# Kernel tuning notes

Measured on AMD Instinct MI355X. Metric: run time of the kernel, lower is better.

## Reference

```python
import jax, jax.numpy as jnp
import numpy as np

N_NODES = 100000
N_EDGES = 3200000


def _gcn_conv(x, src, dst, W, b, n_nodes):
    # PyG GCNConv: out = D^{-1/2} (A + I) D^{-1/2} X W + b
    h = x @ W  # [N, out]
    # degree of (A + I) counted at targets (symmetric graph assumption as in PyG norm)
    deg = jax.ops.segment_sum(jnp.ones_like(dst, dtype=h.dtype), dst, num_segments=n_nodes)
    dinv = jnp.where(deg > 0, jax.lax.rsqrt(deg), 0.0)
    norm = dinv[src] * dinv[dst]  # [E_total]
    msg = h[src] * norm[:, None]  # gather + normalize  [E_total, out]
    out = jax.ops.segment_sum(msg, dst, num_segments=n_nodes)  # scatter-add
    return out + b


def setup_inputs() -> dict:
    key = jax.random.key(0)
    k1, k2, k3, k4 = jax.random.split(key, 4)
    x = jax.random.normal(k1, (N_NODES, 1), dtype=jnp.float32)
    edge_index = jax.random.randint(k2, (2, N_EDGES), 0, N_NODES, dtype=jnp.int64)
    W1 = jax.random.normal(k3, (1, 64), dtype=jnp.float32) * (1.0 / np.sqrt(1.0))
    b1 = jnp.zeros((64,), dtype=jnp.float32)
    W2 = jax.random.normal(k4, (64, 2), dtype=jnp.float32) * (1.0 / np.sqrt(64.0))
    b2 = jnp.zeros((2,), dtype=jnp.float32)
    return {"x": x, "edge_index": edge_index, "W1": W1, "b1": b1, "W2": W2, "b2": b2}


def reference(x, edge_index, W1, b1, W2, b2):
    n = x.shape[0]
    # add self-loops as GCNConv does by default
    loops = jnp.arange(n, dtype=edge_index.dtype)
    src = jnp.concatenate([edge_index[0], loops])
    dst = jnp.concatenate([edge_index[1], loops])
    h = _gcn_conv(x, src, dst, W1, b1, n)
    h = jax.nn.relu(h)
    h = _gcn_conv(h, src, dst, W2, b2, n)
    h = jax.nn.log_softmax(h, axis=1)
    out = jnp.mean(h, axis=0)
    return out[None, :]  # [1, 2]
```

## Files before the change

### kernel.cpp

```cpp
#include <hip/hip_runtime.h>


#define TPB 512
#define SORT_BLK 256
#define BSHIFT 7
#define BNODES 128
#define MAXBUCK 1024
#define BSTRIDE 6144


__global__ __launch_bounds__(TPB) void k_sort(const int* __restrict__ ei, int E, int epb,
                                              int nbuck, int* __restrict__ gcur,
                                              unsigned* __restrict__ packed) {
    __shared__ int h[MAXBUCK];
    for (int b = threadIdx.x; b < nbuck; b += TPB) h[b] = 0;
    __syncthreads();
    const int4* d4 = (const int4*)(ei + E);
    int nq = epb >> 2;
    int q0 = blockIdx.x * nq;
    for (int j = threadIdx.x; j < nq; j += TPB) {
        int q = q0 + j;
        int e = q << 2;
        if (e + 3 < E) {
            int4 v = d4[q];
            atomicAdd(&h[v.x >> BSHIFT], 1);
            atomicAdd(&h[v.y >> BSHIFT], 1);
            atomicAdd(&h[v.z >> BSHIFT], 1);
            atomicAdd(&h[v.w >> BSHIFT], 1);
        } else {
            for (int k = 0; k < 4; ++k)
                if (e + k < E) atomicAdd(&h[(ei + E)[e + k] >> BSHIFT], 1);
        }
    }
    __syncthreads();
    for (int b = threadIdx.x; b < nbuck; b += TPB) {
        int c = h[b];
        h[b] = c ? atomicAdd(&gcur[b], c) : 0;
    }
    __syncthreads();
    const int4* s4 = (const int4*)ei;
    for (int j = threadIdx.x; j < nq; j += TPB) {
        int q = q0 + j;
        int e = q << 2;
        if (e + 3 < E) {
            int4 vs = s4[q];
            int4 vd = d4[q];
            int b, p;
            b = vd.x >> BSHIFT; p = atomicAdd(&h[b], 1);
            packed[b * BSTRIDE + p] = ((unsigned)(vd.x & (BNODES - 1)) << 17) | (unsigned)vs.x;
            b = vd.y >> BSHIFT; p = atomicAdd(&h[b], 1);
            packed[b * BSTRIDE + p] = ((unsigned)(vd.y & (BNODES - 1)) << 17) | (unsigned)vs.y;
            b = vd.z >> BSHIFT; p = atomicAdd(&h[b], 1);
            packed[b * BSTRIDE + p] = ((unsigned)(vd.z & (BNODES - 1)) << 17) | (unsigned)vs.z;
            b = vd.w >> BSHIFT; p = atomicAdd(&h[b], 1);
            packed[b * BSTRIDE + p] = ((unsigned)(vd.w & (BNODES - 1)) << 17) | (unsigned)vs.w;
        } else {
            for (int k = 0; k < 4; ++k) {
                int ee = e + k;
                if (ee < E) {
                    int s = ei[ee], d = ei[E + ee];
                    int b = d >> BSHIFT;
                    int p = atomicAdd(&h[b], 1);
                    packed[b * BSTRIDE + p] = ((unsigned)(d & (BNODES - 1)) << 17) | (unsigned)s;
                }
            }
        }
    }
}


__global__ __launch_bounds__(TPB) void k_csr(unsigned* __restrict__ packed,
                                             const int* __restrict__ gcur,
                                             const float* __restrict__ x,
                                             float* __restrict__ dinv,
                                             float* __restrict__ u,
                                             int* __restrict__ rptr, int N) {
    __shared__ int cnt[8][BNODES];
    __shared__ int eptr[BNODES];
    __shared__ unsigned stage[BSTRIDE];
    for (int k = threadIdx.x; k < 8 * BNODES; k += TPB) ((int*)cnt)[k] = 0;
    __syncthreads();
    int b = blockIdx.x;
    int sz = gcur[b];
    unsigned* base = packed + (size_t)b * BSTRIDE;
    const uint4* base4 = (const uint4*)base;
    int wv = threadIdx.x >> 6;
    int nq4 = sz >> 2;
    int half = nq4 >> 1;
    for (int j = threadIdx.x; j < half; j += TPB) {
        uint4 p = base4[j];
        uint4 q = base4[j + half];
        atomicAdd(&cnt[wv][(p.x >> 17) & 127], 1);
        atomicAdd(&cnt[wv][(p.y >> 17) & 127], 1);
        atomicAdd(&cnt[wv][(p.z >> 17) & 127], 1);
        atomicAdd(&cnt[wv][(p.w >> 17) & 127], 1);
        atomicAdd(&cnt[wv][(q.x >> 17) & 127], 1);
        atomicAdd(&cnt[wv][(q.y >> 17) & 127], 1);
        atomicAdd(&cnt[wv][(q.z >> 17) & 127], 1);
        atomicAdd(&cnt[wv][(q.w >> 17) & 127], 1);
    }
    for (int j = half * 8 + threadIdx.x; j < sz; j += TPB) {
        unsigned p = base[j];
        atomicAdd(&cnt[wv][(p >> 17) & 127], 1);
    }
    __syncthreads();
    int tot = 0;
    if (threadIdx.x < BNODES) {
        #pragma unroll
        for (int c = 0; c < 8; ++c) tot += cnt[c][threadIdx.x];
        eptr[threadIdx.x] = tot;
    }
    __syncthreads();
    for (int d = 1; d < BNODES; d <<= 1) {
        int add = 0;
        if (threadIdx.x < BNODES && threadIdx.x >= d) add = eptr[threadIdx.x - d];
        __syncthreads();
        if (threadIdx.x < BNODES) eptr[threadIdx.x] += add;
        __syncthreads();
    }
    if (threadIdx.x < BNODES) {
        int t = threadIdx.x;
        int ex = eptr[t] - tot;
        int run = ex;
        #pragma unroll
        for (int c = 0; c < 8; ++c) { int v = cnt[c][t]; cnt[c][t] = run; run += v; }
        rptr[b * BNODES + t] = ex;
        int node = (b << BSHIFT) + t;
        if (node < N) {
            float di = rsqrtf((float)(tot + 1));
            dinv[node] = di;
            u[node] = di * x[node];
        }
    }
    __syncthreads();
    for (int j = threadIdx.x; j < half; j += TPB) {
        uint4 p = base4[j];
        uint4 q = base4[j + half];
        int pos;
        pos = atomicAdd(&cnt[wv][(p.x >> 17) & 127], 1); stage[pos] = p.x & 0x1FFFF;
        pos = atomicAdd(&cnt[wv][(p.y >> 17) & 127], 1); stage[pos] = p.y & 0x1FFFF;
        pos = atomicAdd(&cnt[wv][(p.z >> 17) & 127], 1); stage[pos] = p.z & 0x1FFFF;
        pos = atomicAdd(&cnt[wv][(p.w >> 17) & 127], 1); stage[pos] = p.w & 0x1FFFF;
        pos = atomicAdd(&cnt[wv][(q.x >> 17) & 127], 1); stage[pos] = q.x & 0x1FFFF;
        pos = atomicAdd(&cnt[wv][(q.y >> 17) & 127], 1); stage[pos] = q.y & 0x1FFFF;
        pos = atomicAdd(&cnt[wv][(q.z >> 17) & 127], 1); stage[pos] = q.z & 0x1FFFF;
        pos = atomicAdd(&cnt[wv][(q.w >> 17) & 127], 1); stage[pos] = q.w & 0x1FFFF;
    }
    for (int j = half * 8 + threadIdx.x; j < sz; j += TPB) {
        unsigned p = base[j];
        int pos = atomicAdd(&cnt[wv][(p >> 17) & 127], 1);
        stage[pos] = p & 0x1FFFF;
    }
    __syncthreads();
    for (int k = threadIdx.x; k < sz; k += TPB) base[k] = stage[k];
}


__global__ __launch_bounds__(TPB) void k_agg1(const unsigned* __restrict__ sorted,
                                              const int* __restrict__ gcur,
                                              const int* __restrict__ rptr,
                                              const float* __restrict__ dinv,
                                              const float* __restrict__ u,
                                              const float* __restrict__ W1,
                                              const float* __restrict__ b1,
                                              const float* __restrict__ W2,
                                              float2* __restrict__ w, int N) {
    __shared__ float sW1[64], sb1[64], sW2[128];
    __shared__ int sptr[BNODES + 1];
    int b = blockIdx.x;
    if (threadIdx.x < 64) { sW1[threadIdx.x] = W1[threadIdx.x]; sb1[threadIdx.x] = b1[threadIdx.x]; }
    else if (threadIdx.x < 192) sW2[threadIdx.x - 64] = W2[threadIdx.x - 64];
    if (threadIdx.x < BNODES) sptr[threadIdx.x] = rptr[b * BNODES + threadIdx.x];
    if (threadIdx.x == 0) sptr[BNODES] = gcur[b];
    __syncthreads();
    int t = threadIdx.x >> 2, k = threadIdx.x & 3;
    const unsigned* base = sorted + (size_t)b * BSTRIDE;
    int s0 = sptr[t], s1 = sptr[t + 1];
    float s = 0.f;
    int j = s0 + k;
    for (; j + 12 < s1; j += 16) {
        unsigned i0 = base[j], i1 = base[j + 4], i2 = base[j + 8], i3 = base[j + 12];
        float a0 = u[i0], a1 = u[i1], a2 = u[i2], a3 = u[i3];
        s += (a0 + a1) + (a2 + a3);
    }
    for (; j < s1; j += 4) s += u[base[j]];
    s += __shfl_xor(s, 1, 64);
    s += __shfl_xor(s, 2, 64);
    int node = (b << BSHIFT) + t;
    if (k == 0 && node < N) {
        float di = dinv[node];
        float sv = di * (s + u[node]);
        float z0 = 0.f, z1 = 0.f;
        #pragma unroll
        for (int jj = 0; jj < 64; ++jj) {
            float h = fmaxf(fmaf(sv, sW1[jj], sb1[jj]), 0.f);
            z0 = fmaf(h, sW2[2 * jj], z0);
            z1 = fmaf(h, sW2[2 * jj + 1], z1);
        }
        w[node] = make_float2(di * z0, di * z1);
    }
}


__global__ __launch_bounds__(TPB) void k_agg2(const unsigned* __restrict__ sorted,
                                              const int* __restrict__ gcur,
                                              const int* __restrict__ rptr,
                                              const float* __restrict__ dinv,
                                              const float2* __restrict__ w,
                                              const float* __restrict__ b2,
                                              float* __restrict__ accum, int N) {
    __shared__ int sptr[BNODES + 1];
    int b = blockIdx.x;
    if (threadIdx.x < BNODES) sptr[threadIdx.x] = rptr[b * BNODES + threadIdx.x];
    if (threadIdx.x == 0) sptr[BNODES] = gcur[b];
    __syncthreads();
    int t = threadIdx.x >> 2, k = threadIdx.x & 3;
    const unsigned* base = sorted + (size_t)b * BSTRIDE;
    int s0 = sptr[t], s1 = sptr[t + 1];
    float sx = 0.f, sy = 0.f;
    int j = s0 + k;
    for (; j + 12 < s1; j += 16) {
        unsigned i0 = base[j], i1 = base[j + 4], i2 = base[j + 8], i3 = base[j + 12];
        float2 v0 = w[i0], v1 = w[i1], v2 = w[i2], v3 = w[i3];
        sx += (v0.x + v1.x) + (v2.x + v3.x);
        sy += (v0.y + v1.y) + (v2.y + v3.y);
    }
    for (; j < s1; j += 4) {
        float2 v = w[base[j]];
        sx += v.x;
        sy += v.y;
    }
    sx += __shfl_xor(sx, 1, 64); sx += __shfl_xor(sx, 2, 64);
    sy += __shfl_xor(sy, 1, 64); sy += __shfl_xor(sy, 2, 64);
    int node = (b << BSHIFT) + t;
    float l0 = 0.f, l1 = 0.f;
    if (k == 0 && node < N) {
        float di = dinv[node];
        float2 wi = w[node];
        float a0 = di * (sx + wi.x) + b2[0];
        float a1 = di * (sy + wi.y) + b2[1];
        float m = fmaxf(a0, a1);
        float lse = m + logf(expf(a0 - m) + expf(a1 - m));
        l0 = a0 - lse;
        l1 = a1 - lse;
    }
    #pragma unroll
    for (int off = 32; off > 0; off >>= 1) {
        l0 += __shfl_down(l0, off, 64);
        l1 += __shfl_down(l1, off, 64);
    }
    __shared__ float r0[TPB / 64], r1[TPB / 64];
    int wid = threadIdx.x >> 6, lane = threadIdx.x & 63;
    if (lane == 0) { r0[wid] = l0; r1[wid] = l1; }
    __syncthreads();
    if (threadIdx.x == 0) {
        float t0 = 0.f, t1 = 0.f;
        #pragma unroll
        for (int kk = 0; kk < TPB / 64; ++kk) { t0 += r0[kk]; t1 += r1[kk]; }
        accum[2 * b]     = t0;
        accum[2 * b + 1] = t1;
    }
}


#define RTPB 1024
__global__ __launch_bounds__(RTPB) void k_reduce_final(const float* __restrict__ accum,
                                                       int nb, float* __restrict__ out,
                                                       float invN) {
    float t0 = 0.f, t1 = 0.f;
    for (int i = threadIdx.x; i < nb; i += RTPB) {
        t0 += accum[2 * i];
        t1 += accum[2 * i + 1];
    }
    #pragma unroll
    for (int off = 32; off > 0; off >>= 1) {
        t0 += __shfl_down(t0, off, 64);
        t1 += __shfl_down(t1, off, 64);
    }
    __shared__ float s0[RTPB / 64], s1[RTPB / 64];
    int wid = threadIdx.x >> 6, lane = threadIdx.x & 63;
    if (lane == 0) { s0[wid] = t0; s1[wid] = t1; }
    __syncthreads();
    if (threadIdx.x == 0) {
        float a = 0.f, b = 0.f;
        #pragma unroll
        for (int k = 0; k < RTPB / 64; ++k) { a += s0[k]; b += s1[k]; }
        out[0] = a * invN;
        out[1] = b * invN;
    }
}

__global__ void k_finalize(const float* __restrict__ accum, float* __restrict__ out, float invN) {
    out[0] = accum[0] * invN;
    out[1] = accum[1] * invN;
}


#define FTPB 256
__global__ void k_hist(const int* __restrict__ dst, int E, int* __restrict__ deg) {
    int e = blockIdx.x * FTPB + threadIdx.x;
    if (e < E) atomicAdd(&deg[dst[e]], 1);
}
__global__ void k_dinv_u(const int* __restrict__ deg, const float* __restrict__ x,
                         float* __restrict__ dinv, float* __restrict__ u, int N) {
    int i = blockIdx.x * FTPB + threadIdx.x;
    if (i < N) {
        float di = rsqrtf((float)(deg[i] + 1));
        dinv[i] = di;
        u[i] = di * x[i];
    }
}
__global__ void k_scatter1(const int* __restrict__ ei, int E,
                           const float* __restrict__ u, float* __restrict__ t) {
    int e = blockIdx.x * FTPB + threadIdx.x;
    if (e < E) atomicAdd(&t[ei[E + e]], u[ei[e]]);
}
__global__ void k_node_mid_fb(const float* __restrict__ dinv, const float* __restrict__ u,
                              const float* __restrict__ t,
                              const float* __restrict__ W1, const float* __restrict__ b1,
                              const float* __restrict__ W2, float2* __restrict__ w, int N) {
    __shared__ float sW1[64], sb1[64], sW2[128];
    if (threadIdx.x < 64) { sW1[threadIdx.x] = W1[threadIdx.x]; sb1[threadIdx.x] = b1[threadIdx.x]; }
    if (threadIdx.x < 128) sW2[threadIdx.x] = W2[threadIdx.x];
    __syncthreads();
    int i = blockIdx.x * FTPB + threadIdx.x;
    if (i < N) {
        float di = dinv[i];
        float s = di * (t[i] + u[i]);
        float z0 = 0.f, z1 = 0.f;
        #pragma unroll
        for (int j = 0; j < 64; ++j) {
            float h = fmaxf(fmaf(s, sW1[j], sb1[j]), 0.f);
            z0 = fmaf(h, sW2[2 * j], z0);
            z1 = fmaf(h, sW2[2 * j + 1], z1);
        }
        w[i] = make_float2(di * z0, di * z1);
    }
}
__global__ void k_scatter2(const int* __restrict__ ei, int E,
                           const float2* __restrict__ w, float* __restrict__ acc) {
    int e = blockIdx.x * FTPB + threadIdx.x;
    if (e < E) {
        float2 ws = w[ei[e]];
        int d = ei[E + e];
        atomicAdd(&acc[2 * d], ws.x);
        atomicAdd(&acc[2 * d + 1], ws.y);
    }
}
__global__ void k_node_out_fb(const float* __restrict__ dinv, const float2* __restrict__ w,
                              const float2* __restrict__ acc, const float* __restrict__ b2,
                              float* __restrict__ accum, int N) {
    int i = blockIdx.x * FTPB + threadIdx.x;
    float l0 = 0.f, l1 = 0.f;
    if (i < N) {
        float di = dinv[i];
        float2 a = acc[i];
        float2 ww = w[i];
        float a0 = di * (a.x + ww.x) + b2[0];
        float a1 = di * (a.y + ww.y) + b2[1];
        float m = fmaxf(a0, a1);
        float lse = m + logf(expf(a0 - m) + expf(a1 - m));
        l0 = a0 - lse;
        l1 = a1 - lse;
    }
    #pragma unroll
    for (int off = 32; off > 0; off >>= 1) {
        l0 += __shfl_down(l0, off, 64);
        l1 += __shfl_down(l1, off, 64);
    }
    __shared__ float s0[FTPB / 64], s1[FTPB / 64];
    int wid = threadIdx.x >> 6, lane = threadIdx.x & 63;
    if (lane == 0) { s0[wid] = l0; s1[wid] = l1; }
    __syncthreads();
    if (threadIdx.x == 0) {
        float t0 = 0.f, t1 = 0.f;
        #pragma unroll
        for (int k = 0; k < FTPB / 64; ++k) { t0 += s0[k]; t1 += s1[k]; }
        atomicAdd(&accum[0], t0);
        atomicAdd(&accum[1], t1);
    }
}

extern "C" void kernel_launch(void* const* d_in, const int* in_sizes, int n_in,
                              void* d_out, int out_size, void* d_ws, size_t ws_size,
                              hipStream_t stream) {
    const float* x  = (const float*)d_in[0];
    const int*   ei = (const int*)d_in[1];
    const float* W1 = (const float*)d_in[2];
    const float* b1 = (const float*)d_in[3];
    const float* W2 = (const float*)d_in[4];
    const float* b2 = (const float*)d_in[5];
    float* out = (float*)d_out;

    const int N = in_sizes[0];
    const int E = in_sizes[1] / 2;
    const int nbuck = (N + BNODES - 1) >> BSHIFT;
    const int gridN = (N + FTPB - 1) / FTPB;
    const int gridE = (E + FTPB - 1) / FTPB;

    size_t offPacked = 0;
    size_t offW      = offPacked + (size_t)nbuck * BSTRIDE * 4;
    size_t offDinv   = offW + (size_t)N * 8;
    size_t offU      = offDinv + (size_t)N * 4;
    size_t offGcur   = offU + (size_t)N * 4;
    size_t offAccum  = offGcur + (size_t)nbuck * 4;
    size_t offRptr   = offAccum + (size_t)2 * nbuck * 4;
    size_t need      = offRptr + (size_t)nbuck * BNODES * 4;

    if (ws_size >= need && nbuck <= MAXBUCK && N <= (1 << 17)) {
        unsigned* packed = (unsigned*)((char*)d_ws + offPacked);
        float2*   w      = (float2*)((char*)d_ws + offW);
        float*    dinv   = (float*)((char*)d_ws + offDinv);
        float*    u      = (float*)((char*)d_ws + offU);
        int*      gcur   = (int*)((char*)d_ws + offGcur);
        float*    accum  = (float*)((char*)d_ws + offAccum);
        int*      rptr   = (int*)((char*)d_ws + offRptr);

        hipMemsetAsync(gcur, 0, (size_t)nbuck * 4, stream);

        int epb = (((E + SORT_BLK - 1) / SORT_BLK) + 3) & ~3;

        k_sort<<<SORT_BLK, TPB, 0, stream>>>(ei, E, epb, nbuck, gcur, packed);
        k_csr<<<nbuck, TPB, 0, stream>>>(packed, gcur, x, dinv, u, rptr, N);
        k_agg1<<<nbuck, TPB, 0, stream>>>(packed, gcur, rptr, dinv, u, W1, b1, W2, w, N);
        k_agg2<<<nbuck, TPB, 0, stream>>>(packed, gcur, rptr, dinv, (const float2*)w, b2, accum, N);
        k_reduce_final<<<1, RTPB, 0, stream>>>(accum, nbuck, out, 1.0f / (float)N);
    } else {
        int*   deg   = (int*)d_ws;
        float* t     = (float*)(deg + N);
        float* acc   = t + N;
        float* accum = acc + 2 * N;
        float* dinv  = accum + 2;
        float* u     = dinv + N;
        float2* w    = (float2*)(u + N);
        hipMemsetAsync(d_ws, 0, (size_t)(4 * N + 2) * sizeof(float), stream);
        k_hist<<<gridE, FTPB, 0, stream>>>(ei + E, E, deg);
        k_dinv_u<<<gridN, FTPB, 0, stream>>>(deg, x, dinv, u, N);
        k_scatter1<<<gridE, FTPB, 0, stream>>>(ei, E, u, t);
        k_node_mid_fb<<<gridN, FTPB, 0, stream>>>(dinv, u, t, W1, b1, W2, w, N);
        k_scatter2<<<gridE, FTPB, 0, stream>>>(ei, E, w, acc);
        k_node_out_fb<<<gridN, FTPB, 0, stream>>>(dinv, w, (const float2*)acc, b2, accum, N);
        k_finalize<<<1, 64, 0, stream>>>(accum, out, 1.0f / (float)N);
    }
}
```

Before: 160.9 us.

## Cache CSR bucket data in registers, warp-scan offsets, unroll gathers, fuse final reduction

k_csr now loads each bucket's packed edges into registers once and reuses them for both the counting and scatter passes, instead of reading global memory twice. Its 128-entry scan becomes a wavefront shuffle scan, which cuts the many block-wide barriers. The gather loops in both aggregation kernels are unrolled to 8 outstanding loads per lane for more memory-level parallelism. The separate final-reduction kernel is replaced by a last-block-done pattern inside k_agg2, with an atomic counter and fences, which saves one launch but adds atomics and a serial tail in one block.

```diff
diff --git a/kernel.cpp b/kernel.cpp
--- a/kernel.cpp
+++ b/kernel.cpp
@@ -7,6 +7,10 @@
 #define BNODES 128
 #define MAXBUCK 1024
 #define BSTRIDE 6144
+
+__device__ __forceinline__ float ld_dev_f32(const float* p) {
+    return __hip_atomic_load(p, __ATOMIC_RELAXED, __HIP_MEMORY_SCOPE_AGENT);
+}
 
 
 __global__ __launch_bounds__(TPB) void k_sort(const int* __restrict__ ei, int E, int epb,
@@ -78,54 +82,75 @@
     __shared__ int cnt[8][BNODES];
     __shared__ int eptr[BNODES];
     __shared__ unsigned stage[BSTRIDE];
-    for (int k = threadIdx.x; k < 8 * BNODES; k += TPB) ((int*)cnt)[k] = 0;
-    __syncthreads();
-    int b = blockIdx.x;
-    int sz = gcur[b];
+    const int tid = threadIdx.x;
+    for (int k = tid; k < 8 * BNODES; k += TPB) ((int*)cnt)[k] = 0;
+    __syncthreads();
+    const int b = blockIdx.x;
+    const int sz = gcur[b];
     unsigned* base = packed + (size_t)b * BSTRIDE;
     const uint4* base4 = (const uint4*)base;
-    int wv = threadIdx.x >> 6;
-    int nq4 = sz >> 2;
-    int half = nq4 >> 1;
-    for (int j = threadIdx.x; j < half; j += TPB) {
-        uint4 p = base4[j];
-        uint4 q = base4[j + half];
-        atomicAdd(&cnt[wv][(p.x >> 17) & 127], 1);
-        atomicAdd(&cnt[wv][(p.y >> 17) & 127], 1);
-        atomicAdd(&cnt[wv][(p.z >> 17) & 127], 1);
-        atomicAdd(&cnt[wv][(p.w >> 17) & 127], 1);
-        atomicAdd(&cnt[wv][(q.x >> 17) & 127], 1);
-        atomicAdd(&cnt[wv][(q.y >> 17) & 127], 1);
-        atomicAdd(&cnt[wv][(q.z >> 17) & 127], 1);
-        atomicAdd(&cnt[wv][(q.w >> 17) & 127], 1);
-    }
-    for (int j = half * 8 + threadIdx.x; j < sz; j += TPB) {
-        unsigned p = base[j];
-        atomicAdd(&cnt[wv][(p >> 17) & 127], 1);
-    }
+    const int wv = tid >> 6;
+    const int nq4 = sz >> 2;
+    const int half = nq4 >> 1;
+    uint4 rp[2], rq[2];
+    int nit = 0;
+    #pragma unroll
+    for (int it = 0; it < 2; ++it) {
+        int j = tid + it * TPB;
+        if (j < half) {
+            rp[it] = base4[j];
+            rq[it] = base4[j + half];
+            nit = it + 1;
+        }
+    }
+    unsigned rt = 0; int havet = 0;
+    {
+        int j = half * 8 + tid;
+        if (j < sz) { rt = base[j]; havet = 1; }
+    }
+    #pragma unroll
+    for (int it = 0; it < 2; ++it) {
+        if (it < nit) {
+            uint4 p = rp[it], q = rq[it];
+            atomicAdd(&cnt[wv][(p.x >> 17) & 127], 1);
+            atomicAdd(&cnt[wv][(p.y >> 17) & 127], 1);
+            atomicAdd(&cnt[wv][(p.z >> 17) & 127], 1);
+            atomicAdd(&cnt[wv][(p.w >> 17) & 127], 1);
+            atomicAdd(&cnt[wv][(q.x >> 17) & 127], 1);
+            atomicAdd(&cnt[wv][(q.y >> 17) & 127], 1);
+            atomicAdd(&cnt[wv][(q.z >> 17) & 127], 1);
+            atomicAdd(&cnt[wv][(q.w >> 17) & 127], 1);
+        }
+    }
+    if (havet) atomicAdd(&cnt[wv][(rt >> 17) & 127], 1);
     __syncthreads();
     int tot = 0;
-    if (threadIdx.x < BNODES) {
-        #pragma unroll
-        for (int c = 0; c < 8; ++c) tot += cnt[c][threadIdx.x];
-        eptr[threadIdx.x] = tot;
-    }
-    __syncthreads();
-    for (int d = 1; d < BNODES; d <<= 1) {
-        int add = 0;
-        if (threadIdx.x < BNODES && threadIdx.x >= d) add = eptr[threadIdx.x - d];
-        __syncthreads();
-        if (threadIdx.x < BNODES) eptr[threadIdx.x] += add;
-        __syncthreads();
-    }
-    if (threadIdx.x < BNODES) {
-        int t = threadIdx.x;
-        int ex = eptr[t] - tot;
+    if (tid < BNODES) {
+        #pragma unroll
+        for (int c = 0; c < 8; ++c) tot += cnt[c][tid];
+        eptr[tid] = tot;
+    }
+    __syncthreads();
+    if (tid < 64) {
+        int v0 = eptr[tid], v1 = eptr[tid + 64];
+        #pragma unroll
+        for (int off = 1; off < 64; off <<= 1) {
+            int t0 = __shfl_up(v0, off, 64);
+            int t1 = __shfl_up(v1, off, 64);
+            if (tid >= off) { v0 += t0; v1 += t1; }
+        }
+        v1 += __shfl(v0, 63, 64);
+        eptr[tid] = v0;
+        eptr[tid + 64] = v1;
+    }
+    __syncthreads();
+    if (tid < BNODES) {
+        int ex = eptr[tid] - tot;
         int run = ex;
         #pragma unroll
-        for (int c = 0; c < 8; ++c) { int v = cnt[c][t]; cnt[c][t] = run; run += v; }
-        rptr[b * BNODES + t] = ex;
-        int node = (b << BSHIFT) + t;
+        for (int c = 0; c < 8; ++c) { int v = cnt[c][tid]; cnt[c][tid] = run; run += v; }
+        rptr[b * BNODES + tid] = ex;
+        int node = (b << BSHIFT) + tid;
         if (node < N) {
             float di = rsqrtf((float)(tot + 1));
             dinv[node] = di;
@@ -133,26 +158,27 @@
         }
     }
     __syncthreads();
-    for (int j = threadIdx.x; j < half; j += TPB) {
-        uint4 p = base4[j];
-        uint4 q = base4[j + half];
-        int pos;
-        pos = atomicAdd(&cnt[wv][(p.x >> 17) & 127], 1); stage[pos] = p.x & 0x1FFFF;
-        pos = atomicAdd(&cnt[wv][(p.y >> 17) & 127], 1); stage[pos] = p.y & 0x1FFFF;
-        pos = atomicAdd(&cnt[wv][(p.z >> 17) & 127], 1); stage[pos] = p.z & 0x1FFFF;
-        pos = atomicAdd(&cnt[wv][(p.w >> 17) & 127], 1); stage[pos] = p.w & 0x1FFFF;
-        pos = atomicAdd(&cnt[wv][(q.x >> 17) & 127], 1); stage[pos] = q.x & 0x1FFFF;
-        pos = atomicAdd(&cnt[wv][(q.y >> 17) & 127], 1); stage[pos] = q.y & 0x1FFFF;
-        pos = atomicAdd(&cnt[wv][(q.z >> 17) & 127], 1); stage[pos] = q.z & 0x1FFFF;
-        pos = atomicAdd(&cnt[wv][(q.w >> 17) & 127], 1); stage[pos] = q.w & 0x1FFFF;
-    }
-    for (int j = half * 8 + threadIdx.x; j < sz; j += TPB) {
-        unsigned p = base[j];
-        int pos = atomicAdd(&cnt[wv][(p >> 17) & 127], 1);
-        stage[pos] = p & 0x1FFFF;
-    }
-    __syncthreads();
-    for (int k = threadIdx.x; k < sz; k += TPB) base[k] = stage[k];
+    #pragma unroll
+    for (int it = 0; it < 2; ++it) {
+        if (it < nit) {
+            uint4 p = rp[it], q = rq[it];
+            int pos;
+            pos = atomicAdd(&cnt[wv][(p.x >> 17) & 127], 1); stage[pos] = p.x & 0x1FFFF;
+            pos = atomicAdd(&cnt[wv][(p.y >> 17) & 127], 1); stage[pos] = p.y & 0x1FFFF;
+            pos = atomicAdd(&cnt[wv][(p.z >> 17) & 127], 1); stage[pos] = p.z & 0x1FFFF;
+            pos = atomicAdd(&cnt[wv][(p.w >> 17) & 127], 1); stage[pos] = p.w & 0x1FFFF;
+            pos = atomicAdd(&cnt[wv][(q.x >> 17) & 127], 1); stage[pos] = q.x & 0x1FFFF;
+            pos = atomicAdd(&cnt[wv][(q.y >> 17) & 127], 1); stage[pos] = q.y & 0x1FFFF;
+            pos = atomicAdd(&cnt[wv][(q.z >> 17) & 127], 1); stage[pos] = q.z & 0x1FFFF;
+            pos = atomicAdd(&cnt[wv][(q.w >> 17) & 127], 1); stage[pos] = q.w & 0x1FFFF;
+        }
+    }
+    if (havet) {
+        int pos = atomicAdd(&cnt[wv][(rt >> 17) & 127], 1);
+        stage[pos] = rt & 0x1FFFF;
+    }
+    __syncthreads();
+    for (int k = tid; k < sz; k += TPB) base[k] = stage[k];
 }
 
 
@@ -178,6 +204,13 @@
     int s0 = sptr[t], s1 = sptr[t + 1];
     float s = 0.f;
     int j = s0 + k;
+    for (; j + 28 < s1; j += 32) {
+        unsigned i0 = base[j],      i1 = base[j + 4],  i2 = base[j + 8],  i3 = base[j + 12];
+        unsigned i4 = base[j + 16], i5 = base[j + 20], i6 = base[j + 24], i7 = base[j + 28];
+        float a0 = u[i0], a1 = u[i1], a2 = u[i2], a3 = u[i3];
+        float a4 = u[i4], a5 = u[i5], a6 = u[i6], a7 = u[i7];
+        s += ((a0 + a1) + (a2 + a3)) + ((a4 + a5) + (a6 + a7));
+    }
     for (; j + 12 < s1; j += 16) {
         unsigned i0 = base[j], i1 = base[j + 4], i2 = base[j + 8], i3 = base[j + 12];
         float a0 = u[i0], a1 = u[i1], a2 = u[i2], a3 = u[i3];
@@ -208,17 +241,31 @@
                                               const float* __restrict__ dinv,
                                               const float2* __restrict__ w,
                                               const float* __restrict__ b2,
-                                              float* __restrict__ accum, int N) {
+                                              float* __restrict__ accum,
+                                              int* __restrict__ done,
+                                              float* __restrict__ out,
+                                              int nbuck, float invN, int N) {
     __shared__ int sptr[BNODES + 1];
+    __shared__ float r0[TPB / 64], r1[TPB / 64];
+    __shared__ int lastFlag;
+    const int tid = threadIdx.x;
     int b = blockIdx.x;
-    if (threadIdx.x < BNODES) sptr[threadIdx.x] = rptr[b * BNODES + threadIdx.x];
-    if (threadIdx.x == 0) sptr[BNODES] = gcur[b];
-    __syncthreads();
-    int t = threadIdx.x >> 2, k = threadIdx.x & 3;
+    if (tid < BNODES) sptr[tid] = rptr[b * BNODES + tid];
+    if (tid == 0) sptr[BNODES] = gcur[b];
+    __syncthreads();
+    int t = tid >> 2, k = tid & 3;
     const unsigned* base = sorted + (size_t)b * BSTRIDE;
     int s0 = sptr[t], s1 = sptr[t + 1];
     float sx = 0.f, sy = 0.f;
     int j = s0 + k;
+    for (; j + 28 < s1; j += 32) {
+        unsigned i0 = base[j],      i1 = base[j + 4],  i2 = base[j + 8],  i3 = base[j + 12];
+        unsigned i4 = base[j + 16], i5 = base[j + 20], i6 = base[j + 24], i7 = base[j + 28];
+        float2 v0 = w[i0], v1 = w[i1], v2 = w[i2], v3 = w[i3];
+        float2 v4 = w[i4], v5 = w[i5], v6 = w[i6], v7 = w[i7];
+        sx += ((v0.x + v1.x) + (v2.x + v3.x)) + ((v4.x + v5.x) + (v6.x + v7.x));
+        sy += ((v0.y + v1.y) + (v2.y + v3.y)) + ((v4.y + v5.y) + (v6.y + v7.y));
+    }
     for (; j + 12 < s1; j += 16) {
         unsigned i0 = base[j], i1 = base[j + 4], i2 = base[j + 8], i3 = base[j + 12];
         float2 v0 = w[i0], v1 = w[i1], v2 = w[i2], v3 = w[i3];
@@ -249,44 +296,41 @@
         l0 += __shfl_down(l0, off, 64);
         l1 += __shfl_down(l1, off, 64);
     }
-    __shared__ float r0[TPB / 64], r1[TPB / 64];
-    int wid = threadIdx.x >> 6, lane = threadIdx.x & 63;
+    int wid = tid >> 6, lane = tid & 63;
     if (lane == 0) { r0[wid] = l0; r1[wid] = l1; }
     __syncthreads();
-    if (threadIdx.x == 0) {
+    if (tid == 0) {
         float t0 = 0.f, t1 = 0.f;
         #pragma unroll
         for (int kk = 0; kk < TPB / 64; ++kk) { t0 += r0[kk]; t1 += r1[kk]; }
         accum[2 * b]     = t0;
         accum[2 * b + 1] = t1;
-    }
-}
-
-
-#define RTPB 1024
-__global__ __launch_bounds__(RTPB) void k_reduce_final(const float* __restrict__ accum,
-                                                       int nb, float* __restrict__ out,
-                                                       float invN) {
-    float t0 = 0.f, t1 = 0.f;
-    for (int i = threadIdx.x; i < nb; i += RTPB) {
-        t0 += accum[2 * i];
-        t1 += accum[2 * i + 1];
-    }
-    #pragma unroll
-    for (int off = 32; off > 0; off >>= 1) {
-        t0 += __shfl_down(t0, off, 64);
-        t1 += __shfl_down(t1, off, 64);
-    }
-    __shared__ float s0[RTPB / 64], s1[RTPB / 64];
-    int wid = threadIdx.x >> 6, lane = threadIdx.x & 63;
-    if (lane == 0) { s0[wid] = t0; s1[wid] = t1; }
-    __syncthreads();
-    if (threadIdx.x == 0) {
-        float a = 0.f, b = 0.f;
-        #pragma unroll
-        for (int k = 0; k < RTPB / 64; ++k) { a += s0[k]; b += s1[k]; }
-        out[0] = a * invN;
-        out[1] = b * invN;
+        __threadfence();
+        int old = atomicAdd(done, 1);
+        lastFlag = (old == nbuck - 1);
+    }
+    __syncthreads();
+    if (lastFlag) {
+        __threadfence();
+        float t0 = 0.f, t1 = 0.f;
+        for (int i = tid; i < nbuck; i += TPB) {
+            t0 += ld_dev_f32(&accum[2 * i]);
+            t1 += ld_dev_f32(&accum[2 * i + 1]);
+        }
+        #pragma unroll
+        for (int off = 32; off > 0; off >>= 1) {
+            t0 += __shfl_down(t0, off, 64);
+            t1 += __shfl_down(t1, off, 64);
+        }
+        if (lane == 0) { r0[wid] = t0; r1[wid] = t1; }
+        __syncthreads();
+        if (tid == 0) {
+            float a = 0.f, c = 0.f;
+            #pragma unroll
+            for (int kk = 0; kk < TPB / 64; ++kk) { a += r0[kk]; c += r1[kk]; }
+            out[0] = a * invN;
+            out[1] = c * invN;
+        }
     }
 }
 
@@ -403,7 +447,8 @@
     size_t offDinv   = offW + (size_t)N * 8;
     size_t offU      = offDinv + (size_t)N * 4;
     size_t offGcur   = offU + (size_t)N * 4;
-    size_t offAccum  = offGcur + (size_t)nbuck * 4;
+    size_t offDone   = offGcur + (size_t)nbuck * 4;
+    size_t offAccum  = offDone + 4;
     size_t offRptr   = offAccum + (size_t)2 * nbuck * 4;
     size_t need      = offRptr + (size_t)nbuck * BNODES * 4;
 
@@ -413,18 +458,19 @@
         float*    dinv   = (float*)((char*)d_ws + offDinv);
         float*    u      = (float*)((char*)d_ws + offU);
         int*      gcur   = (int*)((char*)d_ws + offGcur);
+        int*      done   = (int*)((char*)d_ws + offDone);
         float*    accum  = (float*)((char*)d_ws + offAccum);
         int*      rptr   = (int*)((char*)d_ws + offRptr);
 
-        hipMemsetAsync(gcur, 0, (size_t)nbuck * 4, stream);
+        hipMemsetAsync(gcur, 0, (size_t)nbuck * 4 + 4, stream);
 
         int epb = (((E + SORT_BLK - 1) / SORT_BLK) + 3) & ~3;
 
         k_sort<<<SORT_BLK, TPB, 0, stream>>>(ei, E, epb, nbuck, gcur, packed);
         k_csr<<<nbuck, TPB, 0, stream>>>(packed, gcur, x, dinv, u, rptr, N);
         k_agg1<<<nbuck, TPB, 0, stream>>>(packed, gcur, rptr, dinv, u, W1, b1, W2, w, N);
-        k_agg2<<<nbuck, TPB, 0, stream>>>(packed, gcur, rptr, dinv, (const float2*)w, b2, accum, N);
-        k_reduce_final<<<1, RTPB, 0, stream>>>(accum, nbuck, out, 1.0f / (float)N);
+        k_agg2<<<nbuck, TPB, 0, stream>>>(packed, gcur, rptr, dinv, (const float2*)w, b2,
+                                          accum, done, out, nbuck, 1.0f / (float)N, N);
     } else {
         int*   deg   = (int*)d_ws;
         float* t     = (float*)(deg + N);
```

New measurement: 174.5 us. +8.4%, slower.
